# Performance work log

Hardware: AMD Instinct MI355X
Metric: run time of the kernel (lower is better)

## Reference

```python
import jax, jax.numpy as jnp
import numpy as np

N = 100000   # num_embeddings
D = 128      # embedding_dims
E = 128      # edge_output_size
S = 2048     # number of streaming interactions
W_DECAY = 1.0  # Decayer w, decay_method='exp': f(dt) = exp(-w*dt)


def setup_inputs() -> dict:
    key = jax.random.key(0)
    ks = jax.random.split(key, 20)
    def nrm(k, shape, s):
        return jax.random.normal(k, shape, jnp.float32) * s
    sD = 1.0 / np.sqrt(D)
    sE = 1.0 / np.sqrt(E)
    return {
        'heads': jax.random.randint(ks[0], (S,), 0, N, dtype=jnp.int32),
        'tails': jax.random.randint(ks[1], (S,), 0, N, dtype=jnp.int32),
        'times': jnp.sort(jax.random.uniform(ks[2], (S,), jnp.float32) * 100.0),
        # node state tables (nn.Embedding weights in the original)
        'node_rep': nrm(ks[3], (N, D), 0.1),
        'cell_head': nrm(ks[4], (N, D), 0.1),
        'hidden_head': nrm(ks[5], (N, D), 0.1),
        'cell_tail': nrm(ks[6], (N, D), 0.1),
        'hidden_tail': nrm(ks[7], (N, D), 0.1),
        # Edge_updater_nn head / tail: act(rep_h @ W1 + rep_t @ W2 + b)
        'Weh1': nrm(ks[8], (D, E), sD), 'Weh2': nrm(ks[9], (D, E), sD), 'beh': jnp.zeros((E,), jnp.float32),
        'Wet1': nrm(ks[10], (D, E), sD), 'Wet2': nrm(ks[11], (D, E), sD), 'bet': jnp.zeros((E,), jnp.float32),
        # TLSTM head (time-decayed LSTM cell)
        'Wxh': nrm(ks[12], (E, 4 * D), sE), 'Whh': nrm(ks[13], (D, 4 * D), sD), 'bh': jnp.zeros((4 * D,), jnp.float32),
        'Wdh': nrm(ks[14], (D, D), sD), 'bdh': jnp.zeros((D,), jnp.float32),
        # TLSTM tail
        'Wxt': nrm(ks[15], (E, 4 * D), sE), 'Wht': nrm(ks[16], (D, 4 * D), sD), 'bt': jnp.zeros((4 * D,), jnp.float32),
        'Wdt': nrm(ks[17], (D, D), sD), 'bdt': jnp.zeros((D,), jnp.float32),
        # Combiner: tanh(h_head @ Wc1 + h_tail @ Wc2)
        'Wc1': nrm(ks[18], (D, D), sD), 'Wc2': nrm(ks[19], (D, D), sD),
    }


def _tlstm(x, c, h, decay, Wx, Wh, b, Wd, bd):
    # Time-aware LSTM: decompose short-term memory, decay it by elapsed time, recombine.
    cs = jnp.tanh(c @ Wd + bd)      # short-term memory component
    c_adj = c - cs + cs * decay      # adjusted previous cell
    z = x @ Wx + h @ Wh + b          # [4D] gate pre-activations
    i, f, o, g = jnp.split(z, 4)
    i = jax.nn.sigmoid(i); f = jax.nn.sigmoid(f); o = jax.nn.sigmoid(o)
    g = jnp.tanh(g)
    c_new = f * c_adj + i * g
    h_new = o * jnp.tanh(c_new)
    return c_new, h_new


def reference(heads, tails, times, node_rep, cell_head, hidden_head, cell_tail, hidden_tail,
              Weh1, Weh2, beh, Wet1, Wet2, bet,
              Wxh, Whh, bh, Wdh, bdh, Wxt, Wht, bt, Wdt, bdt, Wc1, Wc2):
    recent = jnp.zeros((node_rep.shape[0],), jnp.float32)  # recent_timestamp, init 0

    def step(state, ev):
        rep, ch, hh, ct, ht, rt = state
        h_i, t_i, tm = ev
        rep_h = rep[h_i]                    # gather current reps
        rep_t = rep[t_i]
        dec_h = jnp.exp(-W_DECAY * (tm - rt[h_i]))   # decayer(delta_t)
        dec_t = jnp.exp(-W_DECAY * (tm - rt[t_i]))
        edge_h = jnp.tanh(rep_h @ Weh1 + rep_t @ Weh2 + beh)  # edge_updater_head
        edge_t = jnp.tanh(rep_h @ Wet1 + rep_t @ Wet2 + bet)  # edge_updater_tail
        c_h, h_h = _tlstm(edge_h, ch[h_i], hh[h_i], dec_h, Wxh, Whh, bh, Wdh, bdh)
        c_t, h_t = _tlstm(edge_t, ct[t_i], ht[t_i], dec_t, Wxt, Wht, bt, Wdt, bdt)
        new_rep_h = jnp.tanh(h_h @ Wc1 + ht[h_i] @ Wc2)  # combiner(head hidden, tail hidden)
        new_rep_t = jnp.tanh(hh[t_i] @ Wc1 + h_t @ Wc2)
        # scatter updated state (head written before tail, matching original ordering)
        rep = rep.at[h_i].set(new_rep_h).at[t_i].set(new_rep_t)
        ch = ch.at[h_i].set(c_h); hh = hh.at[h_i].set(h_h)
        ct = ct.at[t_i].set(c_t); ht = ht.at[t_i].set(h_t)
        rt = rt.at[h_i].set(tm).at[t_i].set(tm)
        # if_updated=0: emit pre-update representations for this interaction
        return (rep, ch, hh, ct, ht, rt), (rep_h, rep_t)

    state0 = (node_rep, cell_head, hidden_head, cell_tail, hidden_tail, recent)
    _, (out_h, out_t) = jax.lax.scan(step, state0, (heads, tails, times))
    return jnp.stack([out_h, out_t])  # [2, S, D]
```

## Files before the change

kernel.cpp:

```cpp
#include <hip/hip_runtime.h>
#include <hip/hip_cooperative_groups.h>
#include <math.h>

namespace cg = cooperative_groups;

#define DD 128
#define G 8
#define TPB 512
#define SMAX 2048
#define NBLK_MAX 512

__device__ __forceinline__ float sigmoidf(float x) { return 1.0f / (1.0f + expf(-x)); }

struct PParams {
  const int* heads; const int* tails; const float* times;
  float* node_rep; float* cell_head; float* hidden_head; float* cell_tail; float* hidden_tail;
  const float* beh; const float* bet; const float* bh; const float* bt;
  const float* bdh; const float* bdt;
  const float* Wsrc[12];
  float* Wt[12];
  float* out; float* rt;
  int* order; int* level_off; int* n_levels; int* ph; int* pt;
  int S;
};

__global__ __launch_bounds__(TPB, 4) void process_kernel(PParams p) {
  cg::grid_group grid = cg::this_grid();
  const int tid = threadIdx.x;
  const int bid = (int)blockIdx.x;
  const int nb  = (int)gridDim.x;
  const int Sn  = p.S;
  const int b0  = (bid * 7) & 31;

  __shared__ __align__(16) float S_[16384];
  __shared__ int sIdx[G], hIdx[G], tIdx[G];
  __shared__ float tmv[G], decHs[G], decTs[G];
  __shared__ int sh_changed, sh_maxl;

  const int O_REPH = 0,    O_REPT = 1024, O_CHS = 2048, O_CTS = 3072;
  const int O_ZH   = 0,    O_ZT   = 4096;
  const int O_HHS  = 8192, O_HTS  = 9216, O_HTH = 10240, O_HHT = 11264;
  const int O_EH   = 12288, O_ET  = 13312;
  const int O_CAH  = 14336, O_CAT = 15360;

  {
    const int wv = tid >> 6, lane = tid & 63;
    for (int j = bid * 8 + wv; j < Sn; j += nb * 8) {
      const int myh = p.heads[j], myt = p.tails[j];
      int mph = -1, mpt = -1;
      for (int i = lane; i < j; i += 64) {
        int a = p.heads[i], b = p.tails[i];
        if (a == myh || b == myh) mph = i;
        if (a == myt || b == myt) mpt = i;
      }
#pragma unroll
      for (int off = 32; off > 0; off >>= 1) {
        mph = max(mph, __shfl_down(mph, off));
        mpt = max(mpt, __shfl_down(mpt, off));
      }
      if (lane == 0) { p.ph[j] = mph; p.pt[j] = mpt; }
    }
  }

  {
    for (int i = bid * TPB + tid; i < 98304; i += nb * TPB) {
      int mat, k4, e, E;
      if (i < 32768) {
        mat = i >> 12; int rem = i & 4095; k4 = rem >> 7; e = rem & 127; E = 128;
      } else {
        int i2 = i - 32768; mat = 8 + (i2 >> 14); int rem = i2 & 16383;
        k4 = rem >> 9; e = rem & 511; E = 512;
      }
      const float* Wm = p.Wsrc[mat];
      float4 v;
      v.x = Wm[(4 * k4 + 0) * E + e];
      v.y = Wm[(4 * k4 + 1) * E + e];
      v.z = Wm[(4 * k4 + 2) * E + e];
      v.w = Wm[(4 * k4 + 3) * E + e];
      *(float4*)&p.Wt[mat][(size_t)(k4 * E + e) * 4] = v;
    }
  }
  __threadfence();
  grid.sync();

  if (bid == 0) {
    int* lvl = (int*)S_;
    int* ph2 = lvl + SMAX;
    int* pt2 = ph2 + SMAX;
    int* cnt = pt2 + SMAX;
    for (int j = tid; j < Sn; j += TPB) { ph2[j] = p.ph[j]; pt2[j] = p.pt[j]; lvl[j] = 1; }
    __syncthreads();
    for (int it = 0; it < Sn + 2; ++it) {
      if (tid == 0) sh_changed = 0;
      __syncthreads();
      for (int j = tid; j < Sn; j += TPB) {
        int l = 1;
        int a = ph2[j]; if (a >= 0) l = lvl[a] + 1;
        int b = pt2[j]; if (b >= 0) { int lb = lvl[b] + 1; if (lb > l) l = lb; }
        if (l != lvl[j]) { lvl[j] = l; sh_changed = 1; }
      }
      __syncthreads();
      if (!sh_changed) break;
      __syncthreads();
    }
    if (tid == 0) sh_maxl = 0;
    __syncthreads();
    for (int j = tid; j < Sn; j += TPB) atomicMax(&sh_maxl, lvl[j]);
    __syncthreads();
    const int Mlvl = sh_maxl;
    for (int l = tid; l < Mlvl; l += TPB) cnt[l] = 0;
    __syncthreads();
    for (int j = tid; j < Sn; j += TPB) atomicAdd(&cnt[lvl[j] - 1], 1);
    __syncthreads();
    if (tid == 0) {
      int run = 0; p.level_off[0] = 0;
      for (int l = 0; l < Mlvl; ++l) { run += cnt[l]; p.level_off[l + 1] = run; }
      p.n_levels[0] = Mlvl;
    }
    __syncthreads();
    for (int l = tid; l < Mlvl; l += TPB) cnt[l] = 0;
    __syncthreads();
    for (int j = tid; j < Sn; j += TPB) {
      int lv2 = lvl[j] - 1;
      int pos = p.level_off[lv2] + atomicAdd(&cnt[lv2], 1);
      p.order[pos] = j;
    }
  }
  __threadfence();
  grid.sync();

  int nlv = p.n_levels[0];
  if (nlv < 0) nlv = 0;
  if (nlv > SMAX) nlv = SMAX;

  for (int lv = 0; lv < nlv; ++lv) {
    const int beg = p.level_off[lv], end = p.level_off[lv + 1];

    for (int base = beg + bid * G; base < end; base += nb * G) {
      const int ng = min(G, end - base);
      __syncthreads();
      if (tid < ng) {
        int s = p.order[base + tid]; sIdx[tid] = s;
        int h = p.heads[s], t = p.tails[s];
        hIdx[tid] = h; tIdx[tid] = t;
        float tm = p.times[s]; tmv[tid] = tm;
        decHs[tid] = expf(-(tm - p.rt[h]));
        decTs[tid] = expf(-(tm - p.rt[t]));
      }
      __syncthreads();

      {
        const int d = tid & 127;
        for (int g = tid >> 7; g < ng; g += 4) {
          const size_t oh = (size_t)hIdx[g] * DD + d;
          const size_t ot = (size_t)tIdx[g] * DD + d;
          const int b = d * 8 + g;
          float rh = p.node_rep[oh];
          S_[O_REPH + b] = rh; p.out[(size_t)sIdx[g] * DD + d] = rh;
          S_[O_CHS + b] = p.cell_head[oh];
          S_[O_HHS + b] = p.hidden_head[oh];
          S_[O_HTH + b] = p.hidden_tail[oh];
          float rt_ = p.node_rep[ot];
          S_[O_REPT + b] = rt_; p.out[(size_t)(Sn + sIdx[g]) * DD + d] = rt_;
          S_[O_CTS + b] = p.cell_tail[ot];
          S_[O_HTS + b] = p.hidden_tail[ot];
          S_[O_HHT + b] = p.hidden_head[ot];
        }
      }
      __syncthreads();

      {
        const int role = tid >> 7, e = tid & 127;
        if (role <= 1) {
          const float* W1 = p.Wt[role ? 2 : 0];
          const float* W2 = p.Wt[role ? 3 : 1];
          float bv = role ? p.bet[e] : p.beh[e];
          float a[8];
#pragma unroll
          for (int g = 0; g < 8; ++g) a[g] = bv;
#pragma unroll 4
          for (int k4 = 0; k4 < 32; ++k4) {
            const int kk = (k4 + b0) & 31;
            float4 w1 = *(const float4*)&W1[(kk * 128 + e) * 4];
            float4 w2 = *(const float4*)&W2[(kk * 128 + e) * 4];
            const float* w1f = (const float*)&w1;
            const float* w2f = (const float*)&w2;
#pragma unroll
            for (int jj = 0; jj < 4; ++jj) {
              const int d = (kk << 2) + jj;
              const float wa = w1f[jj], wb = w2f[jj];
              float4 rh0 = *(const float4*)&S_[O_REPH + d * 8];
              float4 rh1 = *(const float4*)&S_[O_REPH + d * 8 + 4];
              float4 rt0 = *(const float4*)&S_[O_REPT + d * 8];
              float4 rt1 = *(const float4*)&S_[O_REPT + d * 8 + 4];
              a[0] += rh0.x * wa + rt0.x * wb; a[1] += rh0.y * wa + rt0.y * wb;
              a[2] += rh0.z * wa + rt0.z * wb; a[3] += rh0.w * wa + rt0.w * wb;
              a[4] += rh1.x * wa + rt1.x * wb; a[5] += rh1.y * wa + rt1.y * wb;
              a[6] += rh1.z * wa + rt1.z * wb; a[7] += rh1.w * wa + rt1.w * wb;
            }
          }
          const int dst = role ? O_ET : O_EH;
          float4 o0, o1;
          o0.x = tanhf(a[0]); o0.y = tanhf(a[1]); o0.z = tanhf(a[2]); o0.w = tanhf(a[3]);
          o1.x = tanhf(a[4]); o1.y = tanhf(a[5]); o1.z = tanhf(a[6]); o1.w = tanhf(a[7]);
          *(float4*)&S_[dst + e * 8] = o0;
          *(float4*)&S_[dst + e * 8 + 4] = o1;
        } else {
          const int th = (role == 2);
          const float* W = p.Wt[th ? 4 : 5];
          const int co = th ? O_CHS : O_CTS;
          float bv = th ? p.bdh[e] : p.bdt[e];
          const float* decA = th ? decHs : decTs;
          float a[8];
#pragma unroll
          for (int g = 0; g < 8; ++g) a[g] = bv;
#pragma unroll 4
          for (int k4 = 0; k4 < 32; ++k4) {
            const int kk = (k4 + b0) & 31;
            float4 wd = *(const float4*)&W[(kk * 128 + e) * 4];
            const float* wdf = (const float*)&wd;
#pragma unroll
            for (int jj = 0; jj < 4; ++jj) {
              const int d = (kk << 2) + jj;
              const float wv = wdf[jj];
              float4 c0 = *(const float4*)&S_[co + d * 8];
              float4 c1 = *(const float4*)&S_[co + d * 8 + 4];
              a[0] += c0.x * wv; a[1] += c0.y * wv; a[2] += c0.z * wv; a[3] += c0.w * wv;
              a[4] += c1.x * wv; a[5] += c1.y * wv; a[6] += c1.z * wv; a[7] += c1.w * wv;
            }
          }
          const int dst = th ? O_CAH : O_CAT;
          float o[8];
#pragma unroll
          for (int g = 0; g < 8; ++g) {
            float cs = tanhf(a[g]);
            float c = S_[co + e * 8 + g];
            o[g] = c - cs + cs * decA[g];
          }
          *(float4*)&S_[dst + e * 8]     = make_float4(o[0], o[1], o[2], o[3]);
          *(float4*)&S_[dst + e * 8 + 4] = make_float4(o[4], o[5], o[6], o[7]);
        }
      }
      __syncthreads();

      {
        const int c = tid;
        const float* TXh = p.Wt[8];  const float* THh = p.Wt[9];
        const float* TXt = p.Wt[10]; const float* THt = p.Wt[11];
        float bhv = p.bh[c], btv = p.bt[c];
        float h[8], t8[8];
#pragma unroll
        for (int g = 0; g < 8; ++g) { h[g] = bhv; t8[g] = btv; }
#pragma unroll 2
        for (int k4 = 0; k4 < 32; ++k4) {
          const int kk = (k4 + b0) & 31;
          float4 wxh = *(const float4*)&TXh[(size_t)(kk * 512 + c) * 4];
          float4 whh = *(const float4*)&THh[(size_t)(kk * 512 + c) * 4];
          float4 wxt = *(const float4*)&TXt[(size_t)(kk * 512 + c) * 4];
          float4 wht = *(const float4*)&THt[(size_t)(kk * 512 + c) * 4];
          const float* fxh = (const float*)&wxh;
          const float* fhh = (const float*)&whh;
          const float* fxt = (const float*)&wxt;
          const float* fht = (const float*)&wht;
#pragma unroll
          for (int jj = 0; jj < 4; ++jj) {
            const int d = (kk << 2) + jj;
            float4 ex0 = *(const float4*)&S_[O_EH + d * 8];
            float4 ex1 = *(const float4*)&S_[O_EH + d * 8 + 4];
            float4 hx0 = *(const float4*)&S_[O_HHS + d * 8];
            float4 hx1 = *(const float4*)&S_[O_HHS + d * 8 + 4];
            float4 et0 = *(const float4*)&S_[O_ET + d * 8];
            float4 et1 = *(const float4*)&S_[O_ET + d * 8 + 4];
            float4 ht0 = *(const float4*)&S_[O_HTS + d * 8];
            float4 ht1 = *(const float4*)&S_[O_HTS + d * 8 + 4];
            const float a1 = fxh[jj], a2 = fhh[jj], a3 = fxt[jj], a4 = fht[jj];
            h[0] += ex0.x * a1 + hx0.x * a2; h[1] += ex0.y * a1 + hx0.y * a2;
            h[2] += ex0.z * a1 + hx0.z * a2; h[3] += ex0.w * a1 + hx0.w * a2;
            h[4] += ex1.x * a1 + hx1.x * a2; h[5] += ex1.y * a1 + hx1.y * a2;
            h[6] += ex1.z * a1 + hx1.z * a2; h[7] += ex1.w * a1 + hx1.w * a2;
            t8[0] += et0.x * a3 + ht0.x * a4; t8[1] += et0.y * a3 + ht0.y * a4;
            t8[2] += et0.z * a3 + ht0.z * a4; t8[3] += et0.w * a3 + ht0.w * a4;
            t8[4] += et1.x * a3 + ht1.x * a4; t8[5] += et1.y * a3 + ht1.y * a4;
            t8[6] += et1.z * a3 + ht1.z * a4; t8[7] += et1.w * a3 + ht1.w * a4;
          }
        }
        *(float4*)&S_[O_ZH + c * 8]     = make_float4(h[0], h[1], h[2], h[3]);
        *(float4*)&S_[O_ZH + c * 8 + 4] = make_float4(h[4], h[5], h[6], h[7]);
        *(float4*)&S_[O_ZT + c * 8]     = make_float4(t8[0], t8[1], t8[2], t8[3]);
        *(float4*)&S_[O_ZT + c * 8 + 4] = make_float4(t8[4], t8[5], t8[6], t8[7]);
      }
      __syncthreads();

      {
        const int side = tid >> 8, sub = (tid >> 7) & 1, e2 = tid & 127;
        const int zo = side ? O_ZT : O_ZH;
        const int co = side ? O_CAT : O_CAH;
        const int no = side ? O_ET : O_EH;
        float* ctab = side ? p.cell_tail : p.cell_head;
        float* htab = side ? p.hidden_tail : p.hidden_head;
        for (int q = 0; q < 4; ++q) {
          int g = sub + 2 * q;
          if (g >= ng) continue;
          float iv = sigmoidf(S_[zo + e2 * 8 + g]);
          float fv = sigmoidf(S_[zo + (128 + e2) * 8 + g]);
          float ov = sigmoidf(S_[zo + (256 + e2) * 8 + g]);
          float gv = tanhf(S_[zo + (384 + e2) * 8 + g]);
          float cadj = S_[co + e2 * 8 + g];
          float cn = fv * cadj + iv * gv;
          float hn = ov * tanhf(cn);
          S_[no + e2 * 8 + g] = hn;
          int node = side ? tIdx[g] : hIdx[g];
          ctab[(size_t)node * DD + e2] = cn;
          htab[(size_t)node * DD + e2] = hn;
        }
        if (tid < 2 * G) {
          int g = tid & (G - 1);
          if (g < ng) p.rt[(tid >= G) ? tIdx[g] : hIdx[g]] = tmv[g];
        }
      }
      __syncthreads();

      {
        const int role = tid >> 7, e = tid & 127;
        if (role <= 1) {
          const int xo = role ? O_HHT : O_EH;
          const int yo = role ? O_ET : O_HTH;
          const float* W1 = p.Wt[6];
          const float* W2 = p.Wt[7];
          float a[8];
#pragma unroll
          for (int g = 0; g < 8; ++g) a[g] = 0.f;
#pragma unroll 4
          for (int k4 = 0; k4 < 32; ++k4) {
            const int kk = (k4 + b0) & 31;
            float4 w1 = *(const float4*)&W1[(kk * 128 + e) * 4];
            float4 w2 = *(const float4*)&W2[(kk * 128 + e) * 4];
            const float* w1f = (const float*)&w1;
            const float* w2f = (const float*)&w2;
#pragma unroll
            for (int jj = 0; jj < 4; ++jj) {
              const int d = (kk << 2) + jj;
              const float wa = w1f[jj], wb = w2f[jj];
              float4 x0 = *(const float4*)&S_[xo + d * 8];
              float4 x1 = *(const float4*)&S_[xo + d * 8 + 4];
              float4 y0 = *(const float4*)&S_[yo + d * 8];
              float4 y1 = *(const float4*)&S_[yo + d * 8 + 4];
              a[0] += x0.x * wa + y0.x * wb; a[1] += x0.y * wa + y0.y * wb;
              a[2] += x0.z * wa + y0.z * wb; a[3] += x0.w * wa + y0.w * wb;
              a[4] += x1.x * wa + y1.x * wb; a[5] += x1.y * wa + y1.y * wb;
              a[6] += x1.z * wa + y1.z * wb; a[7] += x1.w * wa + y1.w * wb;
            }
          }
          if (role == 0) {
#pragma unroll
            for (int g = 0; g < 8; ++g)
              if (g < ng && hIdx[g] != tIdx[g])
                p.node_rep[(size_t)hIdx[g] * DD + e] = tanhf(a[g]);
          } else {
#pragma unroll
            for (int g = 0; g < 8; ++g)
              if (g < ng)
                p.node_rep[(size_t)tIdx[g] * DD + e] = tanhf(a[g]);
          }
        }
      }
    }
    __threadfence();
    grid.sync();
  }
}

extern "C" void kernel_launch(void* const* d_in, const int* in_sizes, int n_in,
                              void* d_out, int out_size, void* d_ws, size_t ws_size,
                              hipStream_t stream) {
  const int* heads = (const int*)d_in[0];
  const int* tails = (const int*)d_in[1];
  const float* times = (const float*)d_in[2];
  float* node_rep    = (float*)d_in[3];
  float* cell_head   = (float*)d_in[4];
  float* hidden_head = (float*)d_in[5];
  float* cell_tail   = (float*)d_in[6];
  float* hidden_tail = (float*)d_in[7];

  const int S = in_sizes[0];
  const int N = in_sizes[3] / DD;

  char* ws = (char*)d_ws;
  size_t off = 0;
  float* rt = (float*)ws;
  off = (((size_t)N * 4) + 511) & ~(size_t)511;
  int* order     = (int*)(ws + off); off += (size_t)SMAX * 4;
  int* level_off = (int*)(ws + off); off += (size_t)(SMAX + 1) * 4;
  int* n_levels  = (int*)(ws + off); off += 64 * 4;
  int* ph        = (int*)(ws + off); off += (size_t)SMAX * 4;
  int* pt        = (int*)(ws + off); off += (size_t)SMAX * 4;
  off = (off + 255) & ~(size_t)255;

  PParams p;
  p.heads = heads; p.tails = tails; p.times = times;
  p.node_rep = node_rep; p.cell_head = cell_head; p.hidden_head = hidden_head;
  p.cell_tail = cell_tail; p.hidden_tail = hidden_tail;
  p.beh = (const float*)d_in[10]; p.bet = (const float*)d_in[13];
  p.bh  = (const float*)d_in[16]; p.bt  = (const float*)d_in[21];
  p.bdh = (const float*)d_in[18]; p.bdt = (const float*)d_in[23];
  p.Wsrc[0] = (const float*)d_in[8];
  p.Wsrc[1] = (const float*)d_in[9];
  p.Wsrc[2] = (const float*)d_in[11];
  p.Wsrc[3] = (const float*)d_in[12];
  p.Wsrc[4] = (const float*)d_in[17];
  p.Wsrc[5] = (const float*)d_in[22];
  p.Wsrc[6] = (const float*)d_in[24];
  p.Wsrc[7] = (const float*)d_in[25];
  p.Wsrc[8] = (const float*)d_in[14];
  p.Wsrc[9] = (const float*)d_in[15];
  p.Wsrc[10] = (const float*)d_in[19];
  p.Wsrc[11] = (const float*)d_in[20];

  for (int m = 0; m < 12; ++m) {
    size_t n = (m < 8) ? 16384 : 65536;
    p.Wt[m] = (float*)(ws + off); off += n * 4;
  }

  p.out = (float*)d_out; p.rt = rt;
  p.order = order; p.level_off = level_off; p.n_levels = n_levels;
  p.ph = ph; p.pt = pt;
  p.S = S;

  hipMemsetAsync(rt, 0, (size_t)N * 4, stream);

  void* args[] = { (void*)&p };

  int dev = 0; hipGetDevice(&dev);
  int nCU = 0;
  hipDeviceGetAttribute(&nCU, hipDeviceAttributeMultiprocessorCount, dev);
  if (nCU <= 0) nCU = 256;
  int maxBlkPerCU = 0;
  if (hipOccupancyMaxActiveBlocksPerMultiprocessor(&maxBlkPerCU, process_kernel, TPB, 0)
      != hipSuccess || maxBlkPerCU < 1)
    maxBlkPerCU = 1;
  long long cap = (long long)nCU * (long long)maxBlkPerCU;
  int grid = (int)(cap < NBLK_MAX ? cap : NBLK_MAX);
  if (grid < 1) grid = nCU;

  hipError_t err = hipLaunchCooperativeKernel(process_kernel, dim3(grid), dim3(TPB),
                                              args, 0, stream);
  if (err != hipSuccess && grid > 256) {
    err = hipLaunchCooperativeKernel(process_kernel, dim3(256), dim3(TPB), args, 0, stream);
    grid = 256;
  }
  if (err != hipSuccess && grid > 128) {
    err = hipLaunchCooperativeKernel(process_kernel, dim3(128), dim3(TPB), args, 0, stream);
    grid = 128;
  }
  if (err != hipSuccess && grid > 64) {
    err = hipLaunchCooperativeKernel(process_kernel, dim3(64), dim3(TPB), args, 0, stream);
  }
}
```

Baseline: 748.9 us.

## Use 4x4 register tiles over 16 interactions per block and drop weight transpose

Each block now handles up to 16 independent interactions per level instead of 8. Every GEMV-like stage uses 4 outputs by 4 interactions register tiles that read row-major weights directly as float4. This removes the weight-transpose pre-pass and its workspace, and gives each weight load more reuse. The combiner splits its reduction across two thread halves and merges them through shared memory, which costs an extra barrier. The grid is capped at 256 blocks with doubled shared memory, so fewer blocks run per level and parallelism drops.

New measurement: 790.3 us. 1.06x slower.

```diff
diff --git a/kernel.cpp b/kernel.cpp
--- a/kernel.cpp
+++ b/kernel.cpp
@@ -5,10 +5,10 @@
 namespace cg = cooperative_groups;
 
 #define DD 128
-#define G 8
+#define G 16
 #define TPB 512
 #define SMAX 2048
-#define NBLK_MAX 512
+#define NBLK_MAX 256
 
 __device__ __forceinline__ float sigmoidf(float x) { return 1.0f / (1.0f + expf(-x)); }
 
@@ -17,34 +17,52 @@
   float* node_rep; float* cell_head; float* hidden_head; float* cell_tail; float* hidden_tail;
   const float* beh; const float* bet; const float* bh; const float* bt;
   const float* bdh; const float* bdt;
-  const float* Wsrc[12];
-  float* Wt[12];
+  const float* Weh1; const float* Weh2; const float* Wet1; const float* Wet2;
+  const float* Wdh; const float* Wdt; const float* Wc1; const float* Wc2;
+  const float* Wxh; const float* Whh; const float* Wxt; const float* Wht;
   float* out; float* rt;
   int* order; int* level_off; int* n_levels; int* ph; int* pt;
   int S;
 };
 
-__global__ __launch_bounds__(TPB, 4) void process_kernel(PParams p) {
+#define FMA44_2(A,w1,w2,xa,xb) { \
+  A[0][0]+=(w1).x*(xa).x+(w2).x*(xb).x; A[0][1]+=(w1).x*(xa).y+(w2).x*(xb).y; \
+  A[0][2]+=(w1).x*(xa).z+(w2).x*(xb).z; A[0][3]+=(w1).x*(xa).w+(w2).x*(xb).w; \
+  A[1][0]+=(w1).y*(xa).x+(w2).y*(xb).x; A[1][1]+=(w1).y*(xa).y+(w2).y*(xb).y; \
+  A[1][2]+=(w1).y*(xa).z+(w2).y*(xb).z; A[1][3]+=(w1).y*(xa).w+(w2).y*(xb).w; \
+  A[2][0]+=(w1).z*(xa).x+(w2).z*(xb).x; A[2][1]+=(w1).z*(xa).y+(w2).z*(xb).y; \
+  A[2][2]+=(w1).z*(xa).z+(w2).z*(xb).z; A[2][3]+=(w1).z*(xa).w+(w2).z*(xb).w; \
+  A[3][0]+=(w1).w*(xa).x+(w2).w*(xb).x; A[3][1]+=(w1).w*(xa).y+(w2).w*(xb).y; \
+  A[3][2]+=(w1).w*(xa).z+(w2).w*(xb).z; A[3][3]+=(w1).w*(xa).w+(w2).w*(xb).w; }
+
+#define FMA44_1(A,wv_,xa_) { \
+  A[0][0]+=(wv_).x*(xa_).x; A[0][1]+=(wv_).x*(xa_).y; A[0][2]+=(wv_).x*(xa_).z; A[0][3]+=(wv_).x*(xa_).w; \
+  A[1][0]+=(wv_).y*(xa_).x; A[1][1]+=(wv_).y*(xa_).y; A[1][2]+=(wv_).y*(xa_).z; A[1][3]+=(wv_).y*(xa_).w; \
+  A[2][0]+=(wv_).z*(xa_).x; A[2][1]+=(wv_).z*(xa_).y; A[2][2]+=(wv_).z*(xa_).z; A[2][3]+=(wv_).z*(xa_).w; \
+  A[3][0]+=(wv_).w*(xa_).x; A[3][1]+=(wv_).w*(xa_).y; A[3][2]+=(wv_).w*(xa_).z; A[3][3]+=(wv_).w*(xa_).w; }
+
+__global__ __launch_bounds__(TPB, 2) void process_kernel(PParams p) {
   cg::grid_group grid = cg::this_grid();
   const int tid = threadIdx.x;
   const int bid = (int)blockIdx.x;
   const int nb  = (int)gridDim.x;
   const int Sn  = p.S;
-  const int b0  = (bid * 7) & 31;
-
-  __shared__ __align__(16) float S_[16384];
+  const int wv  = tid >> 6;
+  const int d0  = ((bid * 8 + wv) * 37) & 127;
+
+  __shared__ __align__(16) float S_[32768];
   __shared__ int sIdx[G], hIdx[G], tIdx[G];
   __shared__ float tmv[G], decHs[G], decTs[G];
   __shared__ int sh_changed, sh_maxl;
 
-  const int O_REPH = 0,    O_REPT = 1024, O_CHS = 2048, O_CTS = 3072;
-  const int O_ZH   = 0,    O_ZT   = 4096;
-  const int O_HHS  = 8192, O_HTS  = 9216, O_HTH = 10240, O_HHT = 11264;
-  const int O_EH   = 12288, O_ET  = 13312;
-  const int O_CAH  = 14336, O_CAT = 15360;
+  const int O_REPH = 0,     O_REPT = 2048,  O_CHS = 4096,  O_CTS = 6144;
+  const int O_ZH   = 0,     O_ZT   = 8192;
+  const int O_HHS  = 16384, O_HTS  = 18432, O_HTH = 20480, O_HHT = 22528;
+  const int O_EH   = 24576, O_ET   = 26624;
+  const int O_CAH  = 28672, O_CAT  = 30720;
 
   {
-    const int wv = tid >> 6, lane = tid & 63;
+    const int lane = tid & 63;
     for (int j = bid * 8 + wv; j < Sn; j += nb * 8) {
       const int myh = p.heads[j], myt = p.tails[j];
       int mph = -1, mpt = -1;
@@ -59,25 +77,6 @@
         mpt = max(mpt, __shfl_down(mpt, off));
       }
       if (lane == 0) { p.ph[j] = mph; p.pt[j] = mpt; }
-    }
-  }
-
-  {
-    for (int i = bid * TPB + tid; i < 98304; i += nb * TPB) {
-      int mat, k4, e, E;
-      if (i < 32768) {
-        mat = i >> 12; int rem = i & 4095; k4 = rem >> 7; e = rem & 127; E = 128;
-      } else {
-        int i2 = i - 32768; mat = 8 + (i2 >> 14); int rem = i2 & 16383;
-        k4 = rem >> 9; e = rem & 511; E = 512;
-      }
-      const float* Wm = p.Wsrc[mat];
-      float4 v;
-      v.x = Wm[(4 * k4 + 0) * E + e];
-      v.y = Wm[(4 * k4 + 1) * E + e];
-      v.z = Wm[(4 * k4 + 2) * E + e];
-      v.w = Wm[(4 * k4 + 3) * E + e];
-      *(float4*)&p.Wt[mat][(size_t)(k4 * E + e) * 4] = v;
     }
   }
   __threadfence();
@@ -154,7 +153,7 @@
         for (int g = tid >> 7; g < ng; g += 4) {
           const size_t oh = (size_t)hIdx[g] * DD + d;
           const size_t ot = (size_t)tIdx[g] * DD + d;
-          const int b = d * 8 + g;
+          const int b = d * 16 + g;
           float rh = p.node_rep[oh];
           S_[O_REPH + b] = rh; p.out[(size_t)sIdx[g] * DD + d] = rh;
           S_[O_CHS + b] = p.cell_head[oh];
@@ -170,124 +169,101 @@
       __syncthreads();
 
       {
-        const int role = tid >> 7, e = tid & 127;
+        const int role = tid >> 7;
+        const int r = tid & 127;
+        const int e0 = (r >> 2) * 4;
+        const int g0 = (r & 3) * 4;
         if (role <= 1) {
-          const float* W1 = p.Wt[role ? 2 : 0];
-          const float* W2 = p.Wt[role ? 3 : 1];
-          float bv = role ? p.bet[e] : p.beh[e];
-          float a[8];
-#pragma unroll
-          for (int g = 0; g < 8; ++g) a[g] = bv;
+          const float* W1 = role ? p.Wet1 : p.Weh1;
+          const float* W2 = role ? p.Wet2 : p.Weh2;
+          const float* bias = role ? p.bet : p.beh;
+          float acc[4][4];
+#pragma unroll
+          for (int i = 0; i < 4; ++i) {
+            float bv = bias[e0 + i];
+            acc[i][0] = bv; acc[i][1] = bv; acc[i][2] = bv; acc[i][3] = bv;
+          }
 #pragma unroll 4
-          for (int k4 = 0; k4 < 32; ++k4) {
-            const int kk = (k4 + b0) & 31;
-            float4 w1 = *(const float4*)&W1[(kk * 128 + e) * 4];
-            float4 w2 = *(const float4*)&W2[(kk * 128 + e) * 4];
-            const float* w1f = (const float*)&w1;
-            const float* w2f = (const float*)&w2;
-#pragma unroll
-            for (int jj = 0; jj < 4; ++jj) {
-              const int d = (kk << 2) + jj;
-              const float wa = w1f[jj], wb = w2f[jj];
-              float4 rh0 = *(const float4*)&S_[O_REPH + d * 8];
-              float4 rh1 = *(const float4*)&S_[O_REPH + d * 8 + 4];
-              float4 rt0 = *(const float4*)&S_[O_REPT + d * 8];
-              float4 rt1 = *(const float4*)&S_[O_REPT + d * 8 + 4];
-              a[0] += rh0.x * wa + rt0.x * wb; a[1] += rh0.y * wa + rt0.y * wb;
-              a[2] += rh0.z * wa + rt0.z * wb; a[3] += rh0.w * wa + rt0.w * wb;
-              a[4] += rh1.x * wa + rt1.x * wb; a[5] += rh1.y * wa + rt1.y * wb;
-              a[6] += rh1.z * wa + rt1.z * wb; a[7] += rh1.w * wa + rt1.w * wb;
-            }
+          for (int i = 0; i < 128; ++i) {
+            const int d = (i + d0) & 127;
+            float4 w1 = *(const float4*)&W1[d * 128 + e0];
+            float4 w2 = *(const float4*)&W2[d * 128 + e0];
+            float4 xh = *(const float4*)&S_[O_REPH + d * 16 + g0];
+            float4 xt = *(const float4*)&S_[O_REPT + d * 16 + g0];
+            FMA44_2(acc, w1, w2, xh, xt);
           }
           const int dst = role ? O_ET : O_EH;
-          float4 o0, o1;
-          o0.x = tanhf(a[0]); o0.y = tanhf(a[1]); o0.z = tanhf(a[2]); o0.w = tanhf(a[3]);
-          o1.x = tanhf(a[4]); o1.y = tanhf(a[5]); o1.z = tanhf(a[6]); o1.w = tanhf(a[7]);
-          *(float4*)&S_[dst + e * 8] = o0;
-          *(float4*)&S_[dst + e * 8 + 4] = o1;
+#pragma unroll
+          for (int i = 0; i < 4; ++i)
+            *(float4*)&S_[dst + (e0 + i) * 16 + g0] =
+                make_float4(tanhf(acc[i][0]), tanhf(acc[i][1]),
+                            tanhf(acc[i][2]), tanhf(acc[i][3]));
         } else {
           const int th = (role == 2);
-          const float* W = p.Wt[th ? 4 : 5];
+          const float* W = th ? p.Wdh : p.Wdt;
+          const float* bias = th ? p.bdh : p.bdt;
           const int co = th ? O_CHS : O_CTS;
-          float bv = th ? p.bdh[e] : p.bdt[e];
           const float* decA = th ? decHs : decTs;
-          float a[8];
-#pragma unroll
-          for (int g = 0; g < 8; ++g) a[g] = bv;
+          float acc[4][4];
+#pragma unroll
+          for (int i = 0; i < 4; ++i) {
+            float bv = bias[e0 + i];
+            acc[i][0] = bv; acc[i][1] = bv; acc[i][2] = bv; acc[i][3] = bv;
+          }
 #pragma unroll 4
-          for (int k4 = 0; k4 < 32; ++k4) {
-            const int kk = (k4 + b0) & 31;
-            float4 wd = *(const float4*)&W[(kk * 128 + e) * 4];
-            const float* wdf = (const float*)&wd;
-#pragma unroll
-            for (int jj = 0; jj < 4; ++jj) {
-              const int d = (kk << 2) + jj;
-              const float wv = wdf[jj];
-              float4 c0 = *(const float4*)&S_[co + d * 8];
-              float4 c1 = *(const float4*)&S_[co + d * 8 + 4];
-              a[0] += c0.x * wv; a[1] += c0.y * wv; a[2] += c0.z * wv; a[3] += c0.w * wv;
-              a[4] += c1.x * wv; a[5] += c1.y * wv; a[6] += c1.z * wv; a[7] += c1.w * wv;
-            }
-          }
+          for (int i = 0; i < 128; ++i) {
+            const int d = (i + d0) & 127;
+            float4 wdv = *(const float4*)&W[d * 128 + e0];
+            float4 cv = *(const float4*)&S_[co + d * 16 + g0];
+            FMA44_1(acc, wdv, cv);
+          }
+          const float dv0 = decA[g0], dv1 = decA[g0 + 1],
+                      dv2 = decA[g0 + 2], dv3 = decA[g0 + 3];
           const int dst = th ? O_CAH : O_CAT;
-          float o[8];
-#pragma unroll
-          for (int g = 0; g < 8; ++g) {
-            float cs = tanhf(a[g]);
-            float c = S_[co + e * 8 + g];
-            o[g] = c - cs + cs * decA[g];
-          }
-          *(float4*)&S_[dst + e * 8]     = make_float4(o[0], o[1], o[2], o[3]);
-          *(float4*)&S_[dst + e * 8 + 4] = make_float4(o[4], o[5], o[6], o[7]);
+#pragma unroll
+          for (int i = 0; i < 4; ++i) {
+            float4 cv = *(const float4*)&S_[co + (e0 + i) * 16 + g0];
+            float cs0 = tanhf(acc[i][0]), cs1 = tanhf(acc[i][1]);
+            float cs2 = tanhf(acc[i][2]), cs3 = tanhf(acc[i][3]);
+            *(float4*)&S_[dst + (e0 + i) * 16 + g0] =
+                make_float4(cv.x - cs0 + cs0 * dv0, cv.y - cs1 + cs1 * dv1,
+                            cv.z - cs2 + cs2 * dv2, cv.w - cs3 + cs3 * dv3);
+          }
         }
       }
       __syncthreads();
 
       {
-        const int c = tid;
-        const float* TXh = p.Wt[8];  const float* THh = p.Wt[9];
-        const float* TXt = p.Wt[10]; const float* THt = p.Wt[11];
-        float bhv = p.bh[c], btv = p.bt[c];
-        float h[8], t8[8];
-#pragma unroll
-        for (int g = 0; g < 8; ++g) { h[g] = bhv; t8[g] = btv; }
+        const int c0 = (tid >> 2) * 4;
+        const int g0 = (tid & 3) * 4;
+        float ah[4][4], at[4][4];
+#pragma unroll
+        for (int i = 0; i < 4; ++i) {
+          float bhv = p.bh[c0 + i], btv = p.bt[c0 + i];
+          ah[i][0] = bhv; ah[i][1] = bhv; ah[i][2] = bhv; ah[i][3] = bhv;
+          at[i][0] = btv; at[i][1] = btv; at[i][2] = btv; at[i][3] = btv;
+        }
 #pragma unroll 2
-        for (int k4 = 0; k4 < 32; ++k4) {
-          const int kk = (k4 + b0) & 31;
-          float4 wxh = *(const float4*)&TXh[(size_t)(kk * 512 + c) * 4];
-          float4 whh = *(const float4*)&THh[(size_t)(kk * 512 + c) * 4];
-          float4 wxt = *(const float4*)&TXt[(size_t)(kk * 512 + c) * 4];
-          float4 wht = *(const float4*)&THt[(size_t)(kk * 512 + c) * 4];
-          const float* fxh = (const float*)&wxh;
-          const float* fhh = (const float*)&whh;
-          const float* fxt = (const float*)&wxt;
-          const float* fht = (const float*)&wht;
-#pragma unroll
-          for (int jj = 0; jj < 4; ++jj) {
-            const int d = (kk << 2) + jj;
-            float4 ex0 = *(const float4*)&S_[O_EH + d * 8];
-            float4 ex1 = *(const float4*)&S_[O_EH + d * 8 + 4];
-            float4 hx0 = *(const float4*)&S_[O_HHS + d * 8];
-            float4 hx1 = *(const float4*)&S_[O_HHS + d * 8 + 4];
-            float4 et0 = *(const float4*)&S_[O_ET + d * 8];
-            float4 et1 = *(const float4*)&S_[O_ET + d * 8 + 4];
-            float4 ht0 = *(const float4*)&S_[O_HTS + d * 8];
-            float4 ht1 = *(const float4*)&S_[O_HTS + d * 8 + 4];
-            const float a1 = fxh[jj], a2 = fhh[jj], a3 = fxt[jj], a4 = fht[jj];
-            h[0] += ex0.x * a1 + hx0.x * a2; h[1] += ex0.y * a1 + hx0.y * a2;
-            h[2] += ex0.z * a1 + hx0.z * a2; h[3] += ex0.w * a1 + hx0.w * a2;
-            h[4] += ex1.x * a1 + hx1.x * a2; h[5] += ex1.y * a1 + hx1.y * a2;
-            h[6] += ex1.z * a1 + hx1.z * a2; h[7] += ex1.w * a1 + hx1.w * a2;
-            t8[0] += et0.x * a3 + ht0.x * a4; t8[1] += et0.y * a3 + ht0.y * a4;
-            t8[2] += et0.z * a3 + ht0.z * a4; t8[3] += et0.w * a3 + ht0.w * a4;
-            t8[4] += et1.x * a3 + ht1.x * a4; t8[5] += et1.y * a3 + ht1.y * a4;
-            t8[6] += et1.z * a3 + ht1.z * a4; t8[7] += et1.w * a3 + ht1.w * a4;
-          }
-        }
-        *(float4*)&S_[O_ZH + c * 8]     = make_float4(h[0], h[1], h[2], h[3]);
-        *(float4*)&S_[O_ZH + c * 8 + 4] = make_float4(h[4], h[5], h[6], h[7]);
-        *(float4*)&S_[O_ZT + c * 8]     = make_float4(t8[0], t8[1], t8[2], t8[3]);
-        *(float4*)&S_[O_ZT + c * 8 + 4] = make_float4(t8[4], t8[5], t8[6], t8[7]);
+        for (int i = 0; i < 128; ++i) {
+          const int d = (i + d0) & 127;
+          float4 wxh = *(const float4*)&p.Wxh[d * 512 + c0];
+          float4 whh = *(const float4*)&p.Whh[d * 512 + c0];
+          float4 wxt = *(const float4*)&p.Wxt[d * 512 + c0];
+          float4 wht = *(const float4*)&p.Wht[d * 512 + c0];
+          float4 xe = *(const float4*)&S_[O_EH  + d * 16 + g0];
+          float4 xh = *(const float4*)&S_[O_HHS + d * 16 + g0];
+          float4 fe = *(const float4*)&S_[O_ET  + d * 16 + g0];
+          float4 fh = *(const float4*)&S_[O_HTS + d * 16 + g0];
+          FMA44_2(ah, wxh, whh, xe, xh);
+          FMA44_2(at, wxt, wht, fe, fh);
+        }
+#pragma unroll
+        for (int i = 0; i < 4; ++i) {
+          *(float4*)&S_[O_ZH + (c0 + i) * 16 + g0] =
+              make_float4(ah[i][0], ah[i][1], ah[i][2], ah[i][3]);
+          *(float4*)&S_[O_ZT + (c0 + i) * 16 + g0] =
+              make_float4(at[i][0], at[i][1], at[i][2], at[i][3]);
+        }
       }
       __syncthreads();
 
@@ -298,17 +274,17 @@
         const int no = side ? O_ET : O_EH;
         float* ctab = side ? p.cell_tail : p.cell_head;
         float* htab = side ? p.hidden_tail : p.hidden_head;
-        for (int q = 0; q < 4; ++q) {
+        for (int q = 0; q < 8; ++q) {
           int g = sub + 2 * q;
           if (g >= ng) continue;
-          float iv = sigmoidf(S_[zo + e2 * 8 + g]);
-          float fv = sigmoidf(S_[zo + (128 + e2) * 8 + g]);
-          float ov = sigmoidf(S_[zo + (256 + e2) * 8 + g]);
-          float gv = tanhf(S_[zo + (384 + e2) * 8 + g]);
-          float cadj = S_[co + e2 * 8 + g];
+          float iv = sigmoidf(S_[zo + e2 * 16 + g]);
+          float fv = sigmoidf(S_[zo + (128 + e2) * 16 + g]);
+          float ov = sigmoidf(S_[zo + (256 + e2) * 16 + g]);
+          float gv = tanhf(S_[zo + (384 + e2) * 16 + g]);
+          float cadj = S_[co + e2 * 16 + g];
           float cn = fv * cadj + iv * gv;
           float hn = ov * tanhf(cn);
-          S_[no + e2 * 8 + g] = hn;
+          S_[no + e2 * 16 + g] = hn;
           int node = side ? tIdx[g] : hIdx[g];
           ctab[(size_t)node * DD + e2] = cn;
           htab[(size_t)node * DD + e2] = hn;
@@ -321,46 +297,60 @@
       __syncthreads();
 
       {
-        const int role = tid >> 7, e = tid & 127;
-        if (role <= 1) {
-          const int xo = role ? O_HHT : O_EH;
-          const int yo = role ? O_ET : O_HTH;
-          const float* W1 = p.Wt[6];
-          const float* W2 = p.Wt[7];
-          float a[8];
-#pragma unroll
-          for (int g = 0; g < 8; ++g) a[g] = 0.f;
+        const int role = tid >> 8;
+        const int dh = (tid >> 7) & 1;
+        const int r = tid & 127;
+        const int e0 = (r >> 2) * 4;
+        const int g0 = (r & 3) * 4;
+        const int xo = role ? O_HHT : O_EH;
+        const int yo = role ? O_ET  : O_HTH;
+        const int s0 = dh * 64;
+        float acc[4][4];
+#pragma unroll
+        for (int i = 0; i < 4; ++i) {
+          acc[i][0] = 0.f; acc[i][1] = 0.f; acc[i][2] = 0.f; acc[i][3] = 0.f;
+        }
 #pragma unroll 4
-          for (int k4 = 0; k4 < 32; ++k4) {
-            const int kk = (k4 + b0) & 31;
-            float4 w1 = *(const float4*)&W1[(kk * 128 + e) * 4];
-            float4 w2 = *(const float4*)&W2[(kk * 128 + e) * 4];
-            const float* w1f = (const float*)&w1;
-            const float* w2f = (const float*)&w2;
-#pragma unroll
-            for (int jj = 0; jj < 4; ++jj) {
-              const int d = (kk << 2) + jj;
-              const float wa = w1f[jj], wb = w2f[jj];
-              float4 x0 = *(const float4*)&S_[xo + d * 8];
-              float4 x1 = *(const float4*)&S_[xo + d * 8 + 4];
-              float4 y0 = *(const float4*)&S_[yo + d * 8];
-              float4 y1 = *(const float4*)&S_[yo + d * 8 + 4];
-              a[0] += x0.x * wa + y0.x * wb; a[1] += x0.y * wa + y0.y * wb;
-              a[2] += x0.z * wa + y0.z * wb; a[3] += x0.w * wa + y0.w * wb;
-              a[4] += x1.x * wa + y1.x * wb; a[5] += x1.y * wa + y1.y * wb;
-              a[6] += x1.z * wa + y1.z * wb; a[7] += x1.w * wa + y1.w * wb;
+        for (int i = 0; i < 64; ++i) {
+          const int d = s0 + ((i + d0) & 63);
+          float4 w1 = *(const float4*)&p.Wc1[d * 128 + e0];
+          float4 w2 = *(const float4*)&p.Wc2[d * 128 + e0];
+          float4 xv = *(const float4*)&S_[xo + d * 16 + g0];
+          float4 yv = *(const float4*)&S_[yo + d * 16 + g0];
+          FMA44_2(acc, w1, w2, xv, yv);
+        }
+        const int scr = role ? O_CAT : O_CAH;
+        if (dh == 1) {
+#pragma unroll
+          for (int i = 0; i < 4; ++i)
+            *(float4*)&S_[scr + (e0 + i) * 16 + g0] =
+                make_float4(acc[i][0], acc[i][1], acc[i][2], acc[i][3]);
+        }
+        __syncthreads();
+        if (dh == 0) {
+#pragma unroll
+          for (int i = 0; i < 4; ++i) {
+            float4 pv = *(const float4*)&S_[scr + (e0 + i) * 16 + g0];
+            acc[i][0] += pv.x; acc[i][1] += pv.y; acc[i][2] += pv.z; acc[i][3] += pv.w;
+          }
+#pragma unroll
+          for (int j = 0; j < 4; ++j) {
+            int g = g0 + j;
+            if (g < ng) {
+              if (role == 0) {
+                if (hIdx[g] != tIdx[g]) {
+                  size_t nbase = (size_t)hIdx[g] * DD;
+#pragma unroll
+                  for (int i = 0; i < 4; ++i)
+                    p.node_rep[nbase + e0 + i] = tanhf(acc[i][j]);
+                }
+              } else {
+                size_t nbase = (size_t)tIdx[g] * DD;
+#pragma unroll
+                for (int i = 0; i < 4; ++i)
+                  p.node_rep[nbase + e0 + i] = tanhf(acc[i][j]);
+              }
             }
-          }
-          if (role == 0) {
-#pragma unroll
-            for (int g = 0; g < 8; ++g)
-              if (g < ng && hIdx[g] != tIdx[g])
-                p.node_rep[(size_t)hIdx[g] * DD + e] = tanhf(a[g]);
-          } else {
-#pragma unroll
-            for (int g = 0; g < 8; ++g)
-              if (g < ng)
-                p.node_rep[(size_t)tIdx[g] * DD + e] = tanhf(a[g]);
           }
         }
       }
@@ -394,7 +384,6 @@
   int* n_levels  = (int*)(ws + off); off += 64 * 4;
   int* ph        = (int*)(ws + off); off += (size_t)SMAX * 4;
   int* pt        = (int*)(ws + off); off += (size_t)SMAX * 4;
-  off = (off + 255) & ~(size_t)255;
 
   PParams p;
   p.heads = heads; p.tails = tails; p.times = times;
@@ -403,23 +392,18 @@
   p.beh = (const float*)d_in[10]; p.bet = (const float*)d_in[13];
   p.bh  = (const float*)d_in[16]; p.bt  = (const float*)d_in[21];
   p.bdh = (const float*)d_in[18]; p.bdt = (const float*)d_in[23];
-  p.Wsrc[0] = (const float*)d_in[8];
-  p.Wsrc[1] = (const float*)d_in[9];
-  p.Wsrc[2] = (const float*)d_in[11];
-  p.Wsrc[3] = (const float*)d_in[12];
-  p.Wsrc[4] = (const float*)d_in[17];
-  p.Wsrc[5] = (const float*)d_in[22];
-  p.Wsrc[6] = (const float*)d_in[24];
-  p.Wsrc[7] = (const float*)d_in[25];
-  p.Wsrc[8] = (const float*)d_in[14];
-  p.Wsrc[9] = (const float*)d_in[15];
-  p.Wsrc[10] = (const float*)d_in[19];
-  p.Wsrc[11] = (const float*)d_in[20];
-
-  for (int m = 0; m < 12; ++m) {
-    size_t n = (m < 8) ? 16384 : 65536;
-    p.Wt[m] = (float*)(ws + off); off += n * 4;
-  }
+  p.Weh1 = (const float*)d_in[8];
+  p.Weh2 = (const float*)d_in[9];
+  p.Wet1 = (const float*)d_in[11];
+  p.Wet2 = (const float*)d_in[12];
+  p.Wxh  = (const float*)d_in[14];
+  p.Whh  = (const float*)d_in[15];
+  p.Wdh  = (const float*)d_in[17];
+  p.Wxt  = (const float*)d_in[19];
+  p.Wht  = (const float*)d_in[20];
+  p.Wdt  = (const float*)d_in[22];
+  p.Wc1  = (const float*)d_in[24];
+  p.Wc2  = (const float*)d_in[25];
 
   p.out = (float*)d_out; p.rt = rt;
   p.order = order; p.level_off = level_off; p.n_levels = n_levels;
@@ -444,10 +428,6 @@
 
   hipError_t err = hipLaunchCooperativeKernel(process_kernel, dim3(grid), dim3(TPB),
                                               args, 0, stream);
-  if (err != hipSuccess && grid > 256) {
-    err = hipLaunchCooperativeKernel(process_kernel, dim3(256), dim3(TPB), args, 0, stream);
-    grid = 256;
-  }
   if (err != hipSuccess && grid > 128) {
     err = hipLaunchCooperativeKernel(process_kernel, dim3(128), dim3(TPB), args, 0, stream);
     grid = 128;
```
